# Optimization experiments

Hardware: AMD Instinct MI355X
Metric: run time of the kernel (lower is better)

The kernel has to match this reference:

```python
import jax, jax.numpy as jnp
import numpy as np
import math

FRACTION = 1.0 / math.e  # GOLDEN_ZONE_CENTER


def setup_inputs() -> dict:
    key = jax.random.key(0)
    x = jax.random.normal(key, (4, 4096, 2048), dtype=jnp.float32)
    return {"x": x}


def reference(x) -> jnp.ndarray:
    # Training-mode forward of BoltzmannGateSTE: keep only top-k (k = n/e)
    # activations by global magnitude, zero the rest.
    flat = jnp.abs(x).reshape(-1)
    n = flat.shape[0]
    k = max(1, int(n * FRACTION))  # static python int -> jit-friendly
    if k >= n:
        return x
    topk_vals, _ = jax.lax.top_k(flat, k)
    threshold = topk_vals[-1]  # k-th largest magnitude
    mask = (jnp.abs(x) >= threshold).astype(x.dtype)
    return x * mask
```

## Files before the change

### kernel.cpp

```cpp
#include <hip/hip_runtime.h>
#include <stdint.h>
#include <string.h>


#define SEL_T 1024

constexpr unsigned LO_BITS = 0x3F6147AEu;
constexpr unsigned HI_BITS = 0x3F6B851Fu;
constexpr unsigned NKEY    = HI_BITS - LO_BITS;
constexpr int      NCB     = (NKEY + 1023) / 1024;

constexpr int P_GRID = 4096;
constexpr int P_BLK  = 256;
constexpr int P_WPB  = P_BLK / 64;
constexpr int NWAVES = P_GRID * P_WPB;
constexpr int CAPW   = 128;

constexpr int NBIN1   = 4096;
constexpr int NFINE   = 1 << 19;
constexpr int NCOARSE = 512;
constexpr int F_GRID  = 256;
constexpr int F_BLK   = 256;

#define S_PREF 0
#define S_K1   1
#define S_T    2
#define S_FLAG 3

__device__ __forceinline__ bool gate_skip(const unsigned* state, int gate) {
    if (gate == 0) return false;
    unsigned fl = state[S_FLAG];
    return (gate == 1) ? (fl == 0u) : (fl != 0u);
}

__global__ __launch_bounds__(P_BLK, 8)
void pass_partition(const uint4* __restrict__ x, long long n4,
                    uint4* __restrict__ out, uint2* __restrict__ cand,
                    unsigned* __restrict__ wavecnt, unsigned* __restrict__ blkchi,
                    unsigned* __restrict__ fineH, unsigned* __restrict__ state)
{
    typedef unsigned uv4 __attribute__((ext_vector_type(4)));
    const int lane  = threadIdx.x & 63;
    const int wid   = threadIdx.x >> 6;
    const int gwave = blockIdx.x * P_WPB + wid;
    uint2* my = cand + (size_t)gwave * CAPW;
    const unsigned long long lt = (1ull << lane) - 1ull;

    unsigned wcnt = 0;
    unsigned chi  = 0;
    const long long stride = (long long)gridDim.x * P_BLK;
#pragma unroll 2
    for (long long i = (long long)blockIdx.x * P_BLK + threadIdx.x; i < n4; i += stride) {
        uint4 v = x[i];
        uint4 r;
        unsigned idx0 = (unsigned)(i << 2);
#define DO_COMP(c, off)                                                        \
        { unsigned b = v.c, u = b & 0x7FFFFFFFu;                               \
          bool kp = (u >= HI_BITS);                                            \
          bool cd = (u >= LO_BITS) & !kp;                                      \
          chi += (unsigned)kp;                                                 \
          r.c = kp ? b : 0u;                                                   \
          unsigned long long m = __ballot(cd);                                 \
          if (cd) {                                                            \
              atomicAdd(&fineH[u - LO_BITS], 1u);         \
              unsigned pos = wcnt + (unsigned)__popcll(m & lt);                \
              if (pos < (unsigned)CAPW) my[pos] = make_uint2(b, idx0 + off);   \
          }                                                                    \
          wcnt += (unsigned)__popcll(m); }
        DO_COMP(x, 0) DO_COMP(y, 1) DO_COMP(z, 2) DO_COMP(w, 3)
#undef DO_COMP
        __builtin_nontemporal_store(*(uv4*)&r, (uv4*)(out + i));
    }

    for (int m = 32; m; m >>= 1) chi += __shfl_xor(chi, m, 64);
    __shared__ unsigned s_chi[P_WPB];
    if (lane == 0) {
        s_chi[wid] = chi;
        wavecnt[gwave] = (wcnt < (unsigned)CAPW) ? wcnt : (unsigned)CAPW;
        if (wcnt > (unsigned)CAPW) atomicOr(&state[S_FLAG], 1u);
    }
    __syncthreads();
    if (threadIdx.x == 0) {
        unsigned a = 0;
        for (int w = 0; w < P_WPB; ++w) a += s_chi[w];
        blkchi[blockIdx.x] = a;
    }
}

__global__ __launch_bounds__(64)
void coarse_reduce(const unsigned* __restrict__ fineH, unsigned* __restrict__ coarseH)
{
    unsigned base = blockIdx.x << 10;
    unsigned s = 0;
    for (int t = threadIdx.x; t < 1024; t += 64) {
        unsigned key = base + t;
        s += (key < NKEY) ? fineH[key] : 0u;
    }
    for (int m = 32; m; m >>= 1) s += __shfl_xor(s, m, 64);
    if (threadIdx.x == 0) coarseH[blockIdx.x] = s;
}

__device__ void select_desc(const unsigned* __restrict__ hist, int nbins,
                            unsigned k, unsigned* s_scan, int* s_res)
{
    int tid = threadIdx.x;
    if (tid == 0) { s_res[0] = -1; s_res[1] = 0; }
    __syncthreads();
    unsigned running = 0;
    for (int top = nbins; top > 0; top -= SEL_T) {
        int bin = top - 1 - tid;
        unsigned v = (bin >= 0) ? hist[bin] : 0u;
        s_scan[tid] = v;
        __syncthreads();
        for (int off = 1; off < SEL_T; off <<= 1) {
            unsigned add = (tid >= off) ? s_scan[tid - off] : 0u;
            __syncthreads();
            s_scan[tid] += add;
            __syncthreads();
        }
        unsigned p     = s_scan[tid];
        unsigned pprev = (tid > 0) ? s_scan[tid - 1] : 0u;
        unsigned total = s_scan[SEL_T - 1];
        __syncthreads();
        if (running + total >= k) {
            if (bin >= 0 && running + p >= k && running + pprev < k) {
                s_res[0] = bin;
                s_res[1] = (int)(k - running - pprev);
            }
            __syncthreads();
            return;
        }
        running += total;
    }
    __syncthreads();
}

__global__ __launch_bounds__(SEL_T)
void fast_select(const unsigned* __restrict__ blkchi, const unsigned* __restrict__ wavecnt,
                 const unsigned* __restrict__ coarseH, const unsigned* __restrict__ fineH,
                 unsigned* __restrict__ state, unsigned k)
{
    if (state[S_FLAG]) return;
    __shared__ unsigned s_scan[SEL_T];
    __shared__ int s_res[2];
    __shared__ unsigned long long s_red[SEL_T / 64][2];
    __shared__ unsigned s_kp;
    __shared__ int s_bad;

    unsigned long long chi = 0, tot = 0;
    for (int i = threadIdx.x; i < P_GRID; i += SEL_T) chi += blkchi[i];
    for (int i = threadIdx.x; i < NWAVES; i += SEL_T) tot += wavecnt[i];
    for (int m = 32; m; m >>= 1) {
        chi += __shfl_xor(chi, m, 64);
        tot += __shfl_xor(tot, m, 64);
    }
    int wid = threadIdx.x >> 6, lane = threadIdx.x & 63;
    if (lane == 0) { s_red[wid][0] = chi; s_red[wid][1] = tot; }
    __syncthreads();
    if (threadIdx.x == 0) {
        unsigned long long C = 0, Tt = 0;
        for (int w = 0; w < SEL_T / 64; ++w) { C += s_red[w][0]; Tt += s_red[w][1]; }
        if (C >= (unsigned long long)k || C + Tt < (unsigned long long)k) {
            state[S_FLAG] = 1u;
            s_bad = 1;
        } else { s_bad = 0; s_kp = (unsigned)((unsigned long long)k - C); }
    }
    __syncthreads();
    if (s_bad) return;
    unsigned kp = s_kp;

    select_desc(coarseH, NCB, kp, s_scan, s_res);
    int cb      = s_res[0];
    unsigned r  = (unsigned)s_res[1];
    __syncthreads();
    int nfine = (int)NKEY - cb * 1024;
    if (nfine > 1024) nfine = 1024;
    select_desc(fineH + (size_t)cb * 1024, nfine, r, s_scan, s_res);
    int f = s_res[0];
    if (threadIdx.x == 0)
        state[S_T] = LO_BITS + (unsigned)(cb * 1024 + f);
}

__global__ __launch_bounds__(256)
void cand_fixup(const uint2* __restrict__ cand, const unsigned* __restrict__ state,
                float* __restrict__ out, long long n)
{
    if (state[S_FLAG]) return;
    unsigned T = state[S_T];
    long long total = (long long)NWAVES * CAPW;
    long long stride = (long long)gridDim.x * 256;
    for (long long j = (long long)blockIdx.x * 256 + threadIdx.x; j < total; j += stride) {
        uint2 e = cand[j];
        if ((e.x & 0x7FFFFFFFu) >= T && e.y < (unsigned long long)n)
            out[e.y] = __uint_as_float(e.x);
    }
}

__global__ __launch_bounds__(F_BLK)
void f_hist1(const uint4* __restrict__ x, long long n4, unsigned* __restrict__ histA,
             const unsigned* __restrict__ state, int gate)
{
    if (gate_skip(state, gate)) return;
    __shared__ unsigned h[NBIN1];
    for (int i = threadIdx.x; i < NBIN1; i += F_BLK) h[i] = 0u;
    __syncthreads();
    long long stride = (long long)gridDim.x * F_BLK;
    for (long long i = (long long)blockIdx.x * F_BLK + threadIdx.x; i < n4; i += stride) {
        uint4 v = x[i];
        atomicAdd(&h[(v.x & 0x7FFFFFFFu) >> 19], 1u);
        atomicAdd(&h[(v.y & 0x7FFFFFFFu) >> 19], 1u);
        atomicAdd(&h[(v.z & 0x7FFFFFFFu) >> 19], 1u);
        atomicAdd(&h[(v.w & 0x7FFFFFFFu) >> 19], 1u);
    }
    __syncthreads();
    for (int i = threadIdx.x; i < NBIN1; i += F_BLK)
        if (h[i]) atomicAdd(&histA[i], h[i]);
}

__global__ __launch_bounds__(SEL_T)
void f_select1(const unsigned* __restrict__ histA, unsigned* __restrict__ state,
               unsigned k, int gate)
{
    if (gate_skip(state, gate)) return;
    __shared__ unsigned s_scan[SEL_T];
    __shared__ int s_res[2];
    select_desc(histA, NBIN1, k, s_scan, s_res);
    if (threadIdx.x == 0) {
        state[S_PREF] = (s_res[0] < 0) ? 0u : (unsigned)s_res[0];
        state[S_K1]   = (s_res[0] < 0) ? 1u : (unsigned)s_res[1];
    }
}

__global__ __launch_bounds__(F_BLK)
void f_hist2(const uint4* __restrict__ x, long long n4, const unsigned* __restrict__ state,
             unsigned* __restrict__ fineB, unsigned* __restrict__ coarseB, int gate)
{
    if (gate_skip(state, gate)) return;
    __shared__ unsigned hc[NCOARSE];
    for (int i = threadIdx.x; i < NCOARSE; i += F_BLK) hc[i] = 0u;
    __syncthreads();
    unsigned pref = state[S_PREF];
    long long stride = (long long)gridDim.x * F_BLK;
    for (long long i = (long long)blockIdx.x * F_BLK + threadIdx.x; i < n4; i += stride) {
        uint4 v = x[i];
        unsigned u;
#define DO_C(c) u = v.c & 0x7FFFFFFFu;                                        \
        if ((u >> 19) == pref) {                                              \
            atomicAdd(&fineB[u & (NFINE - 1)], 1u);                           \
            atomicAdd(&hc[(u & (NFINE - 1)) >> 10], 1u); }
        DO_C(x) DO_C(y) DO_C(z) DO_C(w)
#undef DO_C
    }
    __syncthreads();
    for (int i = threadIdx.x; i < NCOARSE; i += F_BLK)
        if (hc[i]) atomicAdd(&coarseB[i], hc[i]);
}

__global__ __launch_bounds__(SEL_T)
void f_select2(const unsigned* __restrict__ fineB, const unsigned* __restrict__ coarseB,
               unsigned* __restrict__ state, int gate)
{
    if (gate_skip(state, gate)) return;
    __shared__ unsigned s_scan[SEL_T];
    __shared__ int s_res[2];
    unsigned pref = state[S_PREF];
    unsigned k    = state[S_K1];
    select_desc(coarseB, NCOARSE, k, s_scan, s_res);
    int c       = (s_res[0] < 0) ? 0 : s_res[0];
    unsigned k1 = (s_res[0] < 0) ? 1u : (unsigned)s_res[1];
    __syncthreads();
    select_desc(fineB + (size_t)c * 1024, 1024, k1, s_scan, s_res);
    int f = (s_res[0] < 0) ? 0 : s_res[0];
    if (threadIdx.x == 0)
        state[S_T] = (pref << 19) | ((unsigned)c << 10) | (unsigned)f;
}

__global__ __launch_bounds__(256)
void f_mask(const uint4* __restrict__ x, uint4* __restrict__ out, long long n4,
            const unsigned* __restrict__ state, int gate)
{
    if (gate_skip(state, gate)) return;
    unsigned t = state[S_T];
    long long stride = (long long)gridDim.x * 256;
    for (long long i = (long long)blockIdx.x * 256 + threadIdx.x; i < n4; i += stride) {
        uint4 v = x[i];
        uint4 r;
        r.x = ((v.x & 0x7FFFFFFFu) >= t) ? v.x : 0u;
        r.y = ((v.y & 0x7FFFFFFFu) >= t) ? v.y : 0u;
        r.z = ((v.z & 0x7FFFFFFFu) >= t) ? v.z : 0u;
        r.w = ((v.w & 0x7FFFFFFFu) >= t) ? v.w : 0u;
        out[i] = r;
    }
}

extern "C" void kernel_launch(void* const* d_in, const int* in_sizes, int n_in,
                              void* d_out, int out_size, void* d_ws, size_t ws_size,
                              hipStream_t stream)
{
    long long n = (long long)in_sizes[0];
    if (n <= 0) return;
    long long n4 = n >> 2;

    const double FRACTION = 1.0 / 2.718281828459045;
    long long k = (long long)((double)n * FRACTION);
    if (k < 1) k = 1;

    const size_t off_state   = 0;
    const size_t off_fineH   = 64;
    const size_t off_coarseH = off_fineH   + (((size_t)NKEY * 4 + 63) & ~63ull);
    const size_t off_fineB   = off_coarseH + (((size_t)NCB * 4 + 63) & ~63ull);
    const size_t off_coarseB = off_fineB   + (size_t)NFINE * 4;
    const size_t off_histA   = off_coarseB + (size_t)NCOARSE * 4;
    const size_t zero_end    = off_histA   + (size_t)NBIN1 * 4;
    const size_t off_wcnt    = zero_end;
    const size_t off_bchi    = off_wcnt + (size_t)NWAVES * 4;
    const size_t off_cand    = off_bchi + (size_t)P_GRID * 4;
    const size_t need_fast   = off_cand + (size_t)NWAVES * CAPW * 8;
    const size_t need_fb     = zero_end;

    uint8_t* base;
    unsigned* state = (unsigned*)d_ws;
    bool fast;
    if (ws_size >= need_fast)     { base = (uint8_t*)d_ws;  fast = true;  }
    else if (ws_size >= need_fb)  { base = (uint8_t*)d_ws;  fast = false; }
    else                          { base = (uint8_t*)d_out; fast = false;
                                    state = (unsigned*)d_ws; }

    unsigned* fineH   = (unsigned*)(base + off_fineH);
    unsigned* coarseH = (unsigned*)(base + off_coarseH);
    unsigned* fineB   = (unsigned*)(base + off_fineB);
    unsigned* coarseB = (unsigned*)(base + off_coarseB);
    unsigned* histA   = (unsigned*)(base + off_histA);
    unsigned* wavecnt = (unsigned*)(base + off_wcnt);
    unsigned* blkchi  = (unsigned*)(base + off_bchi);
    uint2*    cand    = (uint2*)   (base + off_cand);

    const uint4* x = (const uint4*)d_in[0];

    if (fast) {
        hipMemsetAsync(base, 0, zero_end, stream);
        pass_partition<<<P_GRID, P_BLK, 0, stream>>>(x, n4, (uint4*)d_out, cand,
                                                     wavecnt, blkchi, fineH, state);
        coarse_reduce <<<NCB, 64, 0, stream>>>(fineH, coarseH);
        fast_select   <<<1, SEL_T, 0, stream>>>(blkchi, wavecnt, coarseH, fineH,
                                                state, (unsigned)k);
        cand_fixup    <<<512, 256, 0, stream>>>(cand, state, (float*)d_out, n);
        f_hist1  <<<F_GRID, F_BLK, 0, stream>>>(x, n4, histA, state, 1);
        f_select1<<<1, SEL_T, 0, stream>>>(histA, state, (unsigned)k, 1);
        f_hist2  <<<F_GRID, F_BLK, 0, stream>>>(x, n4, state, fineB, coarseB, 1);
        f_select2<<<1, SEL_T, 0, stream>>>(fineB, coarseB, state, 1);
        f_mask   <<<1024, 256, 0, stream>>>(x, (uint4*)d_out, n4, state, 1);
    } else {
        if (state == (unsigned*)d_ws && base != (uint8_t*)d_ws)
            hipMemsetAsync(state, 0, 64, stream);
        hipMemsetAsync(base + off_fineB, 0,
                       ((size_t)NFINE + NCOARSE + NBIN1) * 4, stream);
        if (base == (uint8_t*)d_ws) hipMemsetAsync(state, 0, 64, stream);
        f_hist1  <<<F_GRID, F_BLK, 0, stream>>>(x, n4, histA, state, 0);
        f_select1<<<1, SEL_T, 0, stream>>>(histA, state, (unsigned)k, 0);
        f_hist2  <<<F_GRID, F_BLK, 0, stream>>>(x, n4, state, fineB, coarseB, 0);
        f_select2<<<1, SEL_T, 0, stream>>>(fineB, coarseB, state, 0);
        f_mask   <<<1024, 256, 0, stream>>>(x, (uint4*)d_out, n4, state, 0);
    }
}
```

Measured before the change: 305.1 us.

## Fuse partition, coarse reduce, select and fixup into one cooperative kernel

Replaces the four fast-path kernels (partition pass, coarse histogram reduce, single-block select, candidate fixup) with one cooperative kernel that uses grid.sync between phases. Per-wave candidate lists now live in shared memory, which removes the global candidate buffer and its separate fixup read-back. The grid shrinks to 1024 blocks with a larger per-wave capacity, input loads become nontemporal, and the loop unroll goes up. This saves launch gaps and global traffic, but adds three grid-wide barriers. It also requires every block to be resident at once, which limits occupancy during the streaming phase.

```diff
diff --git a/kernel.cpp b/kernel.cpp
--- a/kernel.cpp
+++ b/kernel.cpp
@@ -1,20 +1,21 @@
 #include <hip/hip_runtime.h>
+#include <hip/hip_cooperative_groups.h>
 #include <stdint.h>
-#include <string.h>
-
-
-#define SEL_T 1024
+
+namespace cg = cooperative_groups;
+
+
+#define SEL_T 256
 
 constexpr unsigned LO_BITS = 0x3F6147AEu;
 constexpr unsigned HI_BITS = 0x3F6B851Fu;
 constexpr unsigned NKEY    = HI_BITS - LO_BITS;
 constexpr int      NCB     = (NKEY + 1023) / 1024;
 
-constexpr int P_GRID = 4096;
+constexpr int P_GRID = 1024;
 constexpr int P_BLK  = 256;
 constexpr int P_WPB  = P_BLK / 64;
-constexpr int NWAVES = P_GRID * P_WPB;
-constexpr int CAPW   = 128;
+constexpr int CAPW   = 512;
 
 constexpr int NBIN1   = 4096;
 constexpr int NFINE   = 1 << 19;
@@ -33,25 +34,71 @@
     return (gate == 1) ? (fl == 0u) : (fl != 0u);
 }
 
-__global__ __launch_bounds__(P_BLK, 8)
-void pass_partition(const uint4* __restrict__ x, long long n4,
-                    uint4* __restrict__ out, uint2* __restrict__ cand,
-                    unsigned* __restrict__ wavecnt, unsigned* __restrict__ blkchi,
-                    unsigned* __restrict__ fineH, unsigned* __restrict__ state)
+__device__ void select_desc(const unsigned* __restrict__ hist, int nbins,
+                            unsigned k, unsigned* s_scan, int* s_res)
+{
+    int tid = threadIdx.x;
+    if (tid == 0) { s_res[0] = -1; s_res[1] = 0; }
+    __syncthreads();
+    unsigned running = 0;
+    for (int top = nbins; top > 0; top -= SEL_T) {
+        int bin = top - 1 - tid;
+        unsigned v = (bin >= 0) ? hist[bin] : 0u;
+        s_scan[tid] = v;
+        __syncthreads();
+        for (int off = 1; off < SEL_T; off <<= 1) {
+            unsigned add = (tid >= off) ? s_scan[tid - off] : 0u;
+            __syncthreads();
+            s_scan[tid] += add;
+            __syncthreads();
+        }
+        unsigned p     = s_scan[tid];
+        unsigned pprev = (tid > 0) ? s_scan[tid - 1] : 0u;
+        unsigned total = s_scan[SEL_T - 1];
+        __syncthreads();
+        if (running + total >= k) {
+            if (bin >= 0 && running + p >= k && running + pprev < k) {
+                s_res[0] = bin;
+                s_res[1] = (int)(k - running - pprev);
+            }
+            __syncthreads();
+            return;
+        }
+        running += total;
+    }
+    __syncthreads();
+}
+
+__global__ __launch_bounds__(P_BLK, 4)
+void fused_fast(const uint4* __restrict__ x, long long n4,
+                uint4* __restrict__ out,
+                unsigned* __restrict__ fineH, unsigned* __restrict__ coarseH,
+                uint2* __restrict__ blkstat, unsigned* __restrict__ state,
+                unsigned k)
 {
     typedef unsigned uv4 __attribute__((ext_vector_type(4)));
-    const int lane  = threadIdx.x & 63;
-    const int wid   = threadIdx.x >> 6;
-    const int gwave = blockIdx.x * P_WPB + wid;
-    uint2* my = cand + (size_t)gwave * CAPW;
+    cg::grid_group grid = cg::this_grid();
+
+    __shared__ uint2 scand[P_WPB][CAPW];
+    __shared__ unsigned s_scan[SEL_T];
+    __shared__ int s_res[2];
+    __shared__ unsigned s_w[P_WPB * 2];
+    __shared__ unsigned long long s_red[P_WPB][2];
+    __shared__ unsigned s_kp;
+    __shared__ int s_bad;
+
+    const int lane = threadIdx.x & 63;
+    const int wid  = threadIdx.x >> 6;
+    uint2* my = scand[wid];
     const unsigned long long lt = (1ull << lane) - 1ull;
 
     unsigned wcnt = 0;
     unsigned chi  = 0;
     const long long stride = (long long)gridDim.x * P_BLK;
-#pragma unroll 2
+#pragma unroll 4
     for (long long i = (long long)blockIdx.x * P_BLK + threadIdx.x; i < n4; i += stride) {
-        uint4 v = x[i];
+        uint4 v;
+        *(uv4*)&v = __builtin_nontemporal_load((const uv4*)(x + i));
         uint4 r;
         unsigned idx0 = (unsigned)(i << 2);
 #define DO_COMP(c, off)                                                        \
@@ -73,126 +120,80 @@
     }
 
     for (int m = 32; m; m >>= 1) chi += __shfl_xor(chi, m, 64);
-    __shared__ unsigned s_chi[P_WPB];
     if (lane == 0) {
-        s_chi[wid] = chi;
-        wavecnt[gwave] = (wcnt < (unsigned)CAPW) ? wcnt : (unsigned)CAPW;
+        s_w[wid]         = chi;
+        s_w[P_WPB + wid] = (wcnt < (unsigned)CAPW) ? wcnt : (unsigned)CAPW;
         if (wcnt > (unsigned)CAPW) atomicOr(&state[S_FLAG], 1u);
     }
     __syncthreads();
     if (threadIdx.x == 0) {
-        unsigned a = 0;
-        for (int w = 0; w < P_WPB; ++w) a += s_chi[w];
-        blkchi[blockIdx.x] = a;
-    }
-}
-
-__global__ __launch_bounds__(64)
-void coarse_reduce(const unsigned* __restrict__ fineH, unsigned* __restrict__ coarseH)
-{
-    unsigned base = blockIdx.x << 10;
-    unsigned s = 0;
-    for (int t = threadIdx.x; t < 1024; t += 64) {
-        unsigned key = base + t;
-        s += (key < NKEY) ? fineH[key] : 0u;
-    }
-    for (int m = 32; m; m >>= 1) s += __shfl_xor(s, m, 64);
-    if (threadIdx.x == 0) coarseH[blockIdx.x] = s;
-}
-
-__device__ void select_desc(const unsigned* __restrict__ hist, int nbins,
-                            unsigned k, unsigned* s_scan, int* s_res)
-{
-    int tid = threadIdx.x;
-    if (tid == 0) { s_res[0] = -1; s_res[1] = 0; }
-    __syncthreads();
-    unsigned running = 0;
-    for (int top = nbins; top > 0; top -= SEL_T) {
-        int bin = top - 1 - tid;
-        unsigned v = (bin >= 0) ? hist[bin] : 0u;
-        s_scan[tid] = v;
-        __syncthreads();
-        for (int off = 1; off < SEL_T; off <<= 1) {
-            unsigned add = (tid >= off) ? s_scan[tid - off] : 0u;
+        unsigned a = 0, b = 0;
+        for (int w = 0; w < P_WPB; ++w) { a += s_w[w]; b += s_w[P_WPB + w]; }
+        blkstat[blockIdx.x] = make_uint2(a, b);
+    }
+
+    grid.sync();
+
+    if (blockIdx.x < (unsigned)NCB) {
+        unsigned base = (unsigned)blockIdx.x << 10;
+        unsigned s = 0;
+        for (int t = threadIdx.x; t < 1024; t += P_BLK) {
+            unsigned key = base + t;
+            s += (key < NKEY) ? fineH[key] : 0u;
+        }
+        for (int m = 32; m; m >>= 1) s += __shfl_xor(s, m, 64);
+        if (lane == 0) s_w[wid] = s;
+        __syncthreads();
+        if (threadIdx.x == 0)
+            coarseH[blockIdx.x] = s_w[0] + s_w[1] + s_w[2] + s_w[3];
+    }
+
+    grid.sync();
+
+    if (blockIdx.x == 0 && state[S_FLAG] == 0) {
+        unsigned long long chiT = 0, totT = 0;
+        for (int i = threadIdx.x; i < P_GRID; i += P_BLK) {
+            uint2 e = blkstat[i]; chiT += e.x; totT += e.y;
+        }
+        for (int m = 32; m; m >>= 1) {
+            chiT += __shfl_xor(chiT, m, 64);
+            totT += __shfl_xor(totT, m, 64);
+        }
+        if (lane == 0) { s_red[wid][0] = chiT; s_red[wid][1] = totT; }
+        __syncthreads();
+        if (threadIdx.x == 0) {
+            unsigned long long C = 0, Tt = 0;
+            for (int w = 0; w < P_WPB; ++w) { C += s_red[w][0]; Tt += s_red[w][1]; }
+            if (C >= (unsigned long long)k || C + Tt < (unsigned long long)k) {
+                state[S_FLAG] = 1u;
+                s_bad = 1;
+            } else { s_bad = 0; s_kp = (unsigned)((unsigned long long)k - C); }
+        }
+        __syncthreads();
+        if (!s_bad) {
+            select_desc(coarseH, NCB, s_kp, s_scan, s_res);
+            int cb      = s_res[0];
+            unsigned r  = (unsigned)s_res[1];
             __syncthreads();
-            s_scan[tid] += add;
-            __syncthreads();
-        }
-        unsigned p     = s_scan[tid];
-        unsigned pprev = (tid > 0) ? s_scan[tid - 1] : 0u;
-        unsigned total = s_scan[SEL_T - 1];
-        __syncthreads();
-        if (running + total >= k) {
-            if (bin >= 0 && running + p >= k && running + pprev < k) {
-                s_res[0] = bin;
-                s_res[1] = (int)(k - running - pprev);
-            }
-            __syncthreads();
-            return;
-        }
-        running += total;
-    }
-    __syncthreads();
-}
-
-__global__ __launch_bounds__(SEL_T)
-void fast_select(const unsigned* __restrict__ blkchi, const unsigned* __restrict__ wavecnt,
-                 const unsigned* __restrict__ coarseH, const unsigned* __restrict__ fineH,
-                 unsigned* __restrict__ state, unsigned k)
-{
-    if (state[S_FLAG]) return;
-    __shared__ unsigned s_scan[SEL_T];
-    __shared__ int s_res[2];
-    __shared__ unsigned long long s_red[SEL_T / 64][2];
-    __shared__ unsigned s_kp;
-    __shared__ int s_bad;
-
-    unsigned long long chi = 0, tot = 0;
-    for (int i = threadIdx.x; i < P_GRID; i += SEL_T) chi += blkchi[i];
-    for (int i = threadIdx.x; i < NWAVES; i += SEL_T) tot += wavecnt[i];
-    for (int m = 32; m; m >>= 1) {
-        chi += __shfl_xor(chi, m, 64);
-        tot += __shfl_xor(tot, m, 64);
-    }
-    int wid = threadIdx.x >> 6, lane = threadIdx.x & 63;
-    if (lane == 0) { s_red[wid][0] = chi; s_red[wid][1] = tot; }
-    __syncthreads();
-    if (threadIdx.x == 0) {
-        unsigned long long C = 0, Tt = 0;
-        for (int w = 0; w < SEL_T / 64; ++w) { C += s_red[w][0]; Tt += s_red[w][1]; }
-        if (C >= (unsigned long long)k || C + Tt < (unsigned long long)k) {
-            state[S_FLAG] = 1u;
-            s_bad = 1;
-        } else { s_bad = 0; s_kp = (unsigned)((unsigned long long)k - C); }
-    }
-    __syncthreads();
-    if (s_bad) return;
-    unsigned kp = s_kp;
-
-    select_desc(coarseH, NCB, kp, s_scan, s_res);
-    int cb      = s_res[0];
-    unsigned r  = (unsigned)s_res[1];
-    __syncthreads();
-    int nfine = (int)NKEY - cb * 1024;
-    if (nfine > 1024) nfine = 1024;
-    select_desc(fineH + (size_t)cb * 1024, nfine, r, s_scan, s_res);
-    int f = s_res[0];
-    if (threadIdx.x == 0)
-        state[S_T] = LO_BITS + (unsigned)(cb * 1024 + f);
-}
-
-__global__ __launch_bounds__(256)
-void cand_fixup(const uint2* __restrict__ cand, const unsigned* __restrict__ state,
-                float* __restrict__ out, long long n)
-{
-    if (state[S_FLAG]) return;
-    unsigned T = state[S_T];
-    long long total = (long long)NWAVES * CAPW;
-    long long stride = (long long)gridDim.x * 256;
-    for (long long j = (long long)blockIdx.x * 256 + threadIdx.x; j < total; j += stride) {
-        uint2 e = cand[j];
-        if ((e.x & 0x7FFFFFFFu) >= T && e.y < (unsigned long long)n)
-            out[e.y] = __uint_as_float(e.x);
+            int nfine = (int)NKEY - cb * 1024;
+            if (nfine > 1024) nfine = 1024;
+            select_desc(fineH + (size_t)cb * 1024, nfine, r, s_scan, s_res);
+            if (threadIdx.x == 0)
+                state[S_T] = LO_BITS + (unsigned)(cb * 1024 + s_res[0]);
+        }
+    }
+
+    grid.sync();
+
+    if (state[S_FLAG] == 0) {
+        unsigned T = state[S_T];
+        unsigned cnt = (wcnt < (unsigned)CAPW) ? wcnt : (unsigned)CAPW;
+        float* outF = (float*)out;
+        for (unsigned j = (unsigned)lane; j < cnt; j += 64) {
+            uint2 e = my[j];
+            if ((e.x & 0x7FFFFFFFu) >= T)
+                outF[e.y] = __uint_as_float(e.x);
+        }
     }
 }
 
@@ -312,10 +313,8 @@
     const size_t off_coarseB = off_fineB   + (size_t)NFINE * 4;
     const size_t off_histA   = off_coarseB + (size_t)NCOARSE * 4;
     const size_t zero_end    = off_histA   + (size_t)NBIN1 * 4;
-    const size_t off_wcnt    = zero_end;
-    const size_t off_bchi    = off_wcnt + (size_t)NWAVES * 4;
-    const size_t off_cand    = off_bchi + (size_t)P_GRID * 4;
-    const size_t need_fast   = off_cand + (size_t)NWAVES * CAPW * 8;
+    const size_t off_blkst   = zero_end;
+    const size_t need_fast   = off_blkst + (size_t)P_GRID * 8;
     const size_t need_fb     = zero_end;
 
     uint8_t* base;
@@ -331,20 +330,26 @@
     unsigned* fineB   = (unsigned*)(base + off_fineB);
     unsigned* coarseB = (unsigned*)(base + off_coarseB);
     unsigned* histA   = (unsigned*)(base + off_histA);
-    unsigned* wavecnt = (unsigned*)(base + off_wcnt);
-    unsigned* blkchi  = (unsigned*)(base + off_bchi);
-    uint2*    cand    = (uint2*)   (base + off_cand);
+    uint2*    blkstat = (uint2*)   (base + off_blkst);
 
     const uint4* x = (const uint4*)d_in[0];
 
     if (fast) {
         hipMemsetAsync(base, 0, zero_end, stream);
-        pass_partition<<<P_GRID, P_BLK, 0, stream>>>(x, n4, (uint4*)d_out, cand,
-                                                     wavecnt, blkchi, fineH, state);
-        coarse_reduce <<<NCB, 64, 0, stream>>>(fineH, coarseH);
-        fast_select   <<<1, SEL_T, 0, stream>>>(blkchi, wavecnt, coarseH, fineH,
-                                                state, (unsigned)k);
-        cand_fixup    <<<512, 256, 0, stream>>>(cand, state, (float*)d_out, n);
+
+        const uint4* xp = x;
+        long long    n4v = n4;
+        uint4*       outp = (uint4*)d_out;
+        unsigned*    fineHp = fineH;
+        unsigned*    coarseHp = coarseH;
+        uint2*       blkstp = blkstat;
+        unsigned*    statep = state;
+        unsigned     kv = (unsigned)k;
+        void* args[] = { (void*)&xp, (void*)&n4v, (void*)&outp, (void*)&fineHp,
+                         (void*)&coarseHp, (void*)&blkstp, (void*)&statep, (void*)&kv };
+        hipLaunchCooperativeKernel((void*)fused_fast, dim3(P_GRID), dim3(P_BLK),
+                                   args, 0, stream);
+
         f_hist1  <<<F_GRID, F_BLK, 0, stream>>>(x, n4, histA, state, 1);
         f_select1<<<1, SEL_T, 0, stream>>>(histA, state, (unsigned)k, 1);
         f_hist2  <<<F_GRID, F_BLK, 0, stream>>>(x, n4, state, fineB, coarseB, 1);
```

After: 618.9 us. 2.03x slower.
